# Optimization experiments

Hardware: AMD Instinct MI355X
Metric: run time of the kernel (lower is better)

The kernel has to match this reference:

```python
import jax, jax.numpy as jnp
import numpy as np

T_STEPS = 64   # fixed number of decode steps (original loops until depot is sampled)
CLIP_C = 10.0  # clip_c init arg


def setup_inputs() -> dict:
    key = jax.random.key(0)
    ks = jax.random.split(key, 8)
    B, N, E = 256, 1024, 256
    s = 0.02
    x = jax.random.normal(ks[0], (B, N, E), jnp.float32)
    demand = jax.random.uniform(ks[1], (B, N), jnp.float32) * 0.1
    demand = demand.at[:, 0].set(0.0)  # depot has zero demand
    capacity0 = jnp.full((B,), 5.0, jnp.float32)
    Wc = jax.random.normal(ks[2], (2 * E + 1, E), jnp.float32) * s
    bc = jnp.zeros((E,), jnp.float32)
    Wqkv = jax.random.normal(ks[3], (E, 3 * E), jnp.float32) * s
    bqkv = jnp.zeros((3 * E,), jnp.float32)
    Wo = jax.random.normal(ks[4], (E, E), jnp.float32) * s
    bo = jnp.zeros((E,), jnp.float32)
    Wpq = jax.random.normal(ks[5], (E, E), jnp.float32) * s
    bpq = jnp.zeros((E,), jnp.float32)
    Wpk = jax.random.normal(ks[6], (E, E), jnp.float32) * s
    bpk = jnp.zeros((E,), jnp.float32)
    return dict(x=x, demand=demand, capacity0=capacity0, Wc=Wc, bc=bc,
                Wqkv=Wqkv, bqkv=bqkv, Wo=Wo, bo=bo,
                Wpq=Wpq, bpq=bpq, Wpk=Wpk, bpk=bpk, num_heads=8)


def _decode(x, demand, capacity0, Wc, bc, Wqkv, bqkv, Wo, bo, Wpq, bpq, Wpk, bpk, num_heads):
    B, N, E = x.shape
    dh = E // num_heads
    scale = np.float32(1.0 / np.sqrt(dh))
    Wq_in, Wk_in, Wv_in = jnp.split(Wqkv, 3, axis=1)
    bq_in, bk_in, bv_in = jnp.split(bqkv, 3)
    # keys/values over static node embeddings: compute once (same math as per-step recompute)
    k_in = (x @ Wk_in + bk_in).reshape(B, N, num_heads, dh)
    v_in = (x @ Wv_in + bv_in).reshape(B, N, num_heads, dh)
    kp = x @ Wpk + bpk  # [B,N,E] pointer keys
    node_ids = jnp.arange(N)

    def step(carry, _):
        visited, current, capacity = carry
        # make_vehicle_embed (torch.no_grad -> stop_gradient)
        w = (~visited).astype(x.dtype)
        mean_embed = jax.lax.stop_gradient((x * w[:, :, None]).sum(1) / w.sum(1, keepdims=True))
        sel = jax.lax.stop_gradient(jnp.take_along_axis(x, current[:, None, None], axis=1)[:, 0])
        cap = jax.lax.stop_gradient(capacity)[:, None]
        ve = jnp.concatenate([mean_embed, sel, cap], axis=1) @ Wc + bc  # [B,E]
        # make_attn_mask: visited or demand > capacity; depot masked while at depot; unmask depot if all masked
        m = visited | (demand > capacity[:, None])
        m = m.at[:, 0].set(jnp.where(current == 0, True, m[:, 0]))
        m = m.at[:, 0].set(jnp.where(jnp.all(m, axis=1), False, m[:, 0]))
        # single-query MHA with key_padding_mask
        q = (ve @ Wq_in + bq_in).reshape(B, num_heads, dh)
        scores = jnp.einsum('bhd,bnhd->bhn', q, k_in) * scale
        attn = jax.nn.softmax(jnp.where(m[:, None, :], -jnp.inf, scores), axis=-1)
        ctx = jnp.einsum('bhn,bnhd->bhd', attn, v_in).reshape(B, E) @ Wo + bo  # [B,E]
        # ProbLayer: clipped-tanh masked softmax
        qp = ctx @ Wpq + bpq
        u = CLIP_C * jnp.tanh(jnp.einsum('bd,bnd->bn', qp, kp))
        prob = jax.nn.softmax(jnp.where(m, -jnp.inf, u), axis=-1)  # [B,N]
        # greedy selection + update_info
        node = jnp.argmax(prob, axis=-1).astype(jnp.int32)
        capacity = capacity - jnp.take_along_axis(demand, node[:, None].astype(jnp.int32), 1)[:, 0]
        visited = visited | ((node_ids[None, :] == node[:, None]) & (node != 0)[:, None])
        return (visited, node, capacity), (prob, node)

    init = (jnp.zeros((B, N), bool), jnp.zeros((B,), jnp.int32), capacity0)
    _, (probs, route) = jax.lax.scan(step, init, None, length=T_STEPS)
    return probs, route  # probs [T,B,N], route [T,B]


def reference(x, demand, capacity0, Wc, bc, Wqkv, bqkv, Wo, bo, Wpq, bpq, Wpk, bpk, num_heads):
    return _decode(x, demand, capacity0, Wc, bc, Wqkv, bqkv, Wo, bo, Wpq, bpq, Wpk, bpk, num_heads)
```

## Files before the change

### kernel.cpp

```cpp
#include <hip/hip_runtime.h>
#include <math.h>

#define BQ 256
#define NN 1024
#define EE 256
#define HH 8
#define TS 64
#define SCALE 0.17677669529663687f
#define CLIPC 10.0f

__global__ __launch_bounds__(256) void init_kernel(
    const float* __restrict__ x, const float* __restrict__ cap0,
    float* __restrict__ sum_embed, float* __restrict__ cnt,
    float* __restrict__ capb, int* __restrict__ curb,
    unsigned char* __restrict__ visited)
{
    int b = blockIdx.x, tid = threadIdx.x;
    #pragma unroll
    for (int i = 0; i < 4; i++) visited[b * NN + tid + i * 256] = 0;
    if (tid == 0) { cnt[b] = 1024.0f; capb[b] = cap0[b]; curb[b] = 0; }
    const float* xb = x + (size_t)b * NN * EE + tid;
    float s = 0.f;
    #pragma unroll 8
    for (int n = 0; n < NN; n++) s += xb[(size_t)n * EE];
    sum_embed[b * EE + tid] = s;
}

__global__ __launch_bounds__(512) void step_kernel(
    const float* __restrict__ x, const float* __restrict__ demand,
    const float* __restrict__ Wc, const float* __restrict__ bc,
    const float* __restrict__ Wqkv, const float* __restrict__ bqkv,
    const float* __restrict__ Wo, const float* __restrict__ bo,
    const float* __restrict__ Wpq, const float* __restrict__ bpq,
    const float* __restrict__ Wpk, const float* __restrict__ bpk,
    float* __restrict__ sum_embed, float* __restrict__ cntb,
    float* __restrict__ capb, int* __restrict__ curb,
    unsigned char* __restrict__ visited,
    float* __restrict__ probs_out, float* __restrict__ route_out, int t)
{
    __shared__ __align__(16) float xs[32768];
    __shared__ __align__(16) float g8[2048];
    __shared__ __align__(16) float ptl[8][16][8];
    __shared__ unsigned char masksh[NN];
    __shared__ float cvec[513];
    __shared__ float vevec[EE];
    __shared__ __align__(16) float qvec[EE];
    __shared__ float ctxv[EE];
    __shared__ float cov[EE];
    __shared__ __align__(16) float qpv[EE];
    __shared__ float uvec[NN];
    __shared__ float skk[512];
    __shared__ float mw_s[64], sw_s[64];
    __shared__ float MM[HH], SS[HH];
    __shared__ float red[8];
    __shared__ int   redi[8];
    __shared__ float s_mx, s_sum, s_ubias;
    __shared__ int   s_node;

    int b = blockIdx.x, tid = threadIdx.x;
    int w = tid >> 6, l = tid & 63;
    float capv = capb[b];
    int cur = curb[b];
    const float* xb = x + (size_t)b * NN * EE;

    {
        uchar2 vis = *(const uchar2*)(visited + b * NN + tid * 2);
        float2 dem = *(const float2*)(demand + b * NN + tid * 2);
        bool m0 = (vis.x != 0) || (dem.x > capv);
        bool m1 = (vis.y != 0) || (dem.y > capv);
        if (tid == 0 && cur == 0) m0 = true;
        masksh[tid * 2]     = m0 ? 1 : 0;
        masksh[tid * 2 + 1] = m1 ? 1 : 0;
        int allm = __syncthreads_and((m0 && m1) ? 1 : 0);
        if (allm && tid == 0) masksh[0] = 0;
    }
    if (tid < EE) {
        cvec[tid]      = sum_embed[b * EE + tid] / cntb[b];
        cvec[EE + tid] = xb[(size_t)cur * EE + tid];
    }
    if (tid == 0) cvec[512] = capv;
    __syncthreads();
    {
        int c = tid & 255, half = tid >> 8;
        int i0 = half * 256, i1 = half ? 513 : 256;
        float acc = 0.f;
        #pragma unroll 8
        for (int i = i0; i < i1; i++) acc = fmaf(cvec[i], Wc[i * EE + c], acc);
        skk[tid] = acc;
        __syncthreads();
        if (tid < EE) vevec[tid] = skk[tid] + skk[256 + tid] + bc[tid];
        __syncthreads();
    }
    {
        int c = tid & 255, half = tid >> 8;
        float acc = 0.f;
        #pragma unroll 8
        for (int i = half * 128; i < half * 128 + 128; i++)
            acc = fmaf(vevec[i], Wqkv[(size_t)i * 768 + c], acc);
        skk[tid] = acc;
        __syncthreads();
        if (tid < EE) qvec[tid] = skk[tid] + skk[256 + tid] + bqkv[tid];
        __syncthreads();
    }
    {
        int e = tid & 255, half = tid >> 8;
        const float* wr = Wqkv + (size_t)e * 768 + 256 + half * 128;
        const float* qh = qvec + half * 128;
        float a4[4] = {0.f, 0.f, 0.f, 0.f};
        #pragma unroll
        for (int k = 0; k < 32; k++) {
            float4 wv = *(const float4*)(wr + k * 4);
            float4 q4 = *(const float4*)(qh + k * 4);
            a4[k >> 3] = fmaf(wv.x, q4.x, fmaf(wv.y, q4.y,
                         fmaf(wv.z, q4.z, fmaf(wv.w, q4.w, a4[k >> 3]))));
        }
        #pragma unroll
        for (int hh2 = 0; hh2 < 4; hh2++)
            g8[(half * 4 + hh2) * EE + e] = SCALE * a4[hh2];
    }
    __syncthreads();

    float* xw = xs + w * 4096;
    int qtr = l >> 4, r = l & 15;
    float wsv[8][4] = {};
    float mrun[8], srun[8];
    #pragma unroll
    for (int h = 0; h < 8; h++) { mrun[h] = -INFINITY; srun[h] = 0.f; }

    for (int tt = 0; tt < 8; tt++) {
        int n0 = (w + tt * 8) * 16;
        float4 stg[16];
        #pragma unroll
        for (int i = 0; i < 16; i++)
            stg[i] = *(const float4*)(xb + (size_t)(n0 + i) * EE + l * 4);
        #pragma unroll
        for (int i = 0; i < 16; i++)
            *(float4*)(xw + i * 256 + ((l ^ (i & 7)) << 2)) = stg[i];
        float sacc[8] = {0.f, 0.f, 0.f, 0.f, 0.f, 0.f, 0.f, 0.f};
        #pragma unroll
        for (int gi = 0; gi < 16; gi++) {
            int c = qtr * 16 + ((gi + 2 * qtr) & 15);
            float4 xv = *(const float4*)(xw + r * 256 + ((c ^ (r & 7)) << 2));
            #pragma unroll
            for (int h = 0; h < 8; h++) {
                float4 gv = *(const float4*)(g8 + h * EE + (c << 2));
                sacc[h] = fmaf(xv.x, gv.x, fmaf(xv.y, gv.y,
                          fmaf(xv.z, gv.z, fmaf(xv.w, gv.w, sacc[h]))));
            }
        }
        int n = n0 + r;
        bool msk = masksh[n] != 0;
        float ptv[8], fac[8];
        #pragma unroll
        for (int h = 0; h < 8; h++) {
            float v = sacc[h];
            v += __shfl_xor(v, 16);
            v += __shfl_xor(v, 32);
            v = msk ? -INFINITY : v;
            float tm = v;
            tm = fmaxf(tm, __shfl_xor(tm, 1));
            tm = fmaxf(tm, __shfl_xor(tm, 2));
            tm = fmaxf(tm, __shfl_xor(tm, 4));
            tm = fmaxf(tm, __shfl_xor(tm, 8));
            float mo = mrun[h];
            float mn = fmaxf(mo, tm);
            float f  = (mo == -INFINITY) ? 0.f : expf(mo - mn);
            float pt = msk ? 0.f : expf(v - mn);
            float tsum = pt;
            tsum += __shfl_xor(tsum, 1);
            tsum += __shfl_xor(tsum, 2);
            tsum += __shfl_xor(tsum, 4);
            tsum += __shfl_xor(tsum, 8);
            srun[h] = fmaf(srun[h], f, tsum);
            mrun[h] = mn;
            fac[h] = f; ptv[h] = pt;
        }
        #pragma unroll
        for (int h = 0; h < 8; h++) {
            wsv[h][0] *= fac[h]; wsv[h][1] *= fac[h];
            wsv[h][2] *= fac[h]; wsv[h][3] *= fac[h];
        }
        if (qtr == 0) {
            *(float4*)&ptl[w][r][0] = make_float4(ptv[0], ptv[1], ptv[2], ptv[3]);
            *(float4*)&ptl[w][r][4] = make_float4(ptv[4], ptv[5], ptv[6], ptv[7]);
        }
        #pragma unroll
        for (int nd = 0; nd < 16; nd++) {
            float4 xv = *(const float4*)(xw + nd * 256 + ((l ^ (nd & 7)) << 2));
            float4 pa = *(const float4*)&ptl[w][nd][0];
            float4 pb = *(const float4*)&ptl[w][nd][4];
#define WSACC(H, P) \
            wsv[H][0] = fmaf(P, xv.x, wsv[H][0]); \
            wsv[H][1] = fmaf(P, xv.y, wsv[H][1]); \
            wsv[H][2] = fmaf(P, xv.z, wsv[H][2]); \
            wsv[H][3] = fmaf(P, xv.w, wsv[H][3]);
            WSACC(0, pa.x) WSACC(1, pa.y) WSACC(2, pa.z) WSACC(3, pa.w)
            WSACC(4, pb.x) WSACC(5, pb.y) WSACC(6, pb.z) WSACC(7, pb.w)
#undef WSACC
        }
    }
    if (l == 0) {
        #pragma unroll
        for (int h = 0; h < 8; h++) { mw_s[w * 8 + h] = mrun[h]; sw_s[w * 8 + h] = srun[h]; }
    }
    __syncthreads();
    if (tid < 8) {
        float M = -INFINITY;
        for (int w2 = 0; w2 < 8; w2++) M = fmaxf(M, mw_s[w2 * 8 + tid]);
        float S = 0.f;
        for (int w2 = 0; w2 < 8; w2++) {
            float mm = mw_s[w2 * 8 + tid];
            if (mm > -INFINITY) S += sw_s[w2 * 8 + tid] * expf(mm - M);
        }
        MM[tid] = M; SS[tid] = S;
    }
    __syncthreads();
    #pragma unroll
    for (int h = 0; h < 8; h++) {
        float mm = mrun[h];
        float f = (mm > -INFINITY) ? expf(mm - MM[h]) : 0.f;
        *(float4*)(xs + (w * 8 + h) * 256 + l * 4) =
            make_float4(wsv[h][0] * f, wsv[h][1] * f, wsv[h][2] * f, wsv[h][3] * f);
    }
    __syncthreads();
    #pragma unroll
    for (int k = 0; k < 4; k++) {
        int idx = tid + k * 512;
        float s = 0.f;
        #pragma unroll
        for (int w2 = 0; w2 < 8; w2++) s += xs[w2 * 2048 + idx];
        g8[idx] = s;
    }
    __syncthreads();

    {
        int c = tid & 255, half = tid >> 8;
        int h2 = c >> 5;
        const float* wv = Wqkv + 512 + c;
        float acc = 0.f;
        #pragma unroll 8
        for (int e = half * 128; e < half * 128 + 128; e++)
            acc = fmaf(g8[h2 * EE + e], wv[(size_t)e * 768], acc);
        skk[tid] = acc;
        __syncthreads();
        if (tid < EE) ctxv[tid] = (skk[tid] + skk[256 + tid]) / SS[tid >> 5] + bqkv[512 + tid];
        __syncthreads();
    }
    {
        int c = tid & 255, half = tid >> 8;
        float acc = 0.f;
        #pragma unroll 8
        for (int i = half * 128; i < half * 128 + 128; i++)
            acc = fmaf(ctxv[i], Wo[(size_t)i * EE + c], acc);
        skk[tid] = acc;
        __syncthreads();
        if (tid < EE) cov[tid] = skk[tid] + skk[256 + tid] + bo[tid];
        __syncthreads();
    }
    {
        int c = tid & 255, half = tid >> 8;
        float acc = 0.f;
        #pragma unroll 8
        for (int i = half * 128; i < half * 128 + 128; i++)
            acc = fmaf(cov[i], Wpq[(size_t)i * EE + c], acc);
        skk[tid] = acc;
        __syncthreads();
        if (tid < EE) qpv[tid] = skk[tid] + skk[256 + tid] + bpq[tid];
        __syncthreads();
    }
    {
        float v = (tid < EE) ? qpv[tid] * bpk[tid] : 0.f;
        #pragma unroll
        for (int o = 32; o > 0; o >>= 1) v += __shfl_down(v, o);
        if (l == 0) red[w] = v;
        __syncthreads();
        if (tid == 0) {
            float s2 = 0.f;
            for (int i = 0; i < 8; i++) s2 += red[i];
            s_ubias = s2;
        }
    }
    {
        __syncthreads();
        int e = tid & 255, half = tid >> 8;
        const float* wr = Wpk + (size_t)e * EE + half * 128;
        const float* qh = qpv + half * 128;
        float acc = 0.f;
        #pragma unroll
        for (int k = 0; k < 32; k++) {
            float4 wv = *(const float4*)(wr + k * 4);
            float4 q4 = *(const float4*)(qh + k * 4);
            acc = fmaf(wv.x, q4.x, fmaf(wv.y, q4.y,
                  fmaf(wv.z, q4.z, fmaf(wv.w, q4.w, acc))));
        }
        skk[tid] = acc;
        __syncthreads();
        if (tid < EE) g8[tid] = skk[tid] + skk[256 + tid];
        __syncthreads();
    }

    float ubias = s_ubias;
    for (int tt = 0; tt < 8; tt++) {
        int n0 = (w + tt * 8) * 16;
        float4 stg[16];
        #pragma unroll
        for (int i = 0; i < 16; i++)
            stg[i] = *(const float4*)(xb + (size_t)(n0 + i) * EE + l * 4);
        #pragma unroll
        for (int i = 0; i < 16; i++)
            *(float4*)(xw + i * 256 + ((l ^ (i & 7)) << 2)) = stg[i];
        float acc = 0.f;
        #pragma unroll
        for (int gi = 0; gi < 16; gi++) {
            int c = qtr * 16 + ((gi + 2 * qtr) & 15);
            float4 xv = *(const float4*)(xw + r * 256 + ((c ^ (r & 7)) << 2));
            float4 hv = *(const float4*)(g8 + (c << 2));
            acc = fmaf(xv.x, hv.x, fmaf(xv.y, hv.y,
                  fmaf(xv.z, hv.z, fmaf(xv.w, hv.w, acc))));
        }
        acc += __shfl_xor(acc, 16);
        acc += __shfl_xor(acc, 32);
        if (qtr == 0) {
            int n = n0 + r;
            uvec[n] = masksh[n] ? -INFINITY : CLIPC * tanhf(acc + ubias);
        }
    }
    __syncthreads();

    float u0 = uvec[tid], u1 = uvec[tid + 512];
    float lmax = fmaxf(u0, u1);
    #pragma unroll
    for (int o = 32; o > 0; o >>= 1) lmax = fmaxf(lmax, __shfl_down(lmax, o));
    if (l == 0) red[w] = lmax;
    __syncthreads();
    if (tid == 0) {
        float m2 = red[0];
        for (int i = 1; i < 8; i++) m2 = fmaxf(m2, red[i]);
        s_mx = m2;
    }
    __syncthreads();
    float mx = s_mx;
    float p0 = (u0 == -INFINITY) ? 0.f : expf(u0 - mx);
    float p1 = (u1 == -INFINITY) ? 0.f : expf(u1 - mx);
    float ls = p0 + p1;
    #pragma unroll
    for (int o = 32; o > 0; o >>= 1) ls += __shfl_down(ls, o);
    if (l == 0) red[w] = ls;
    __syncthreads();
    if (tid == 0) {
        float s2 = 0.f;
        for (int i = 0; i < 8; i++) s2 += red[i];
        s_sum = s2;
    }
    __syncthreads();
    float sm = s_sum;
    p0 = p0 / sm; p1 = p1 / sm;
    size_t pbase = (size_t)t * BQ * NN + (size_t)b * NN;
    probs_out[pbase + tid] = p0;
    probs_out[pbase + tid + 512] = p1;
    float bu; int bn;
    if (p1 > p0) { bu = p1; bn = tid + 512; } else { bu = p0; bn = tid; }
    #pragma unroll
    for (int o = 32; o > 0; o >>= 1) {
        float ou = __shfl_down(bu, o);
        int   on = __shfl_down(bn, o);
        if (ou > bu || (ou == bu && on < bn)) { bu = ou; bn = on; }
    }
    if (l == 0) { red[w] = bu; redi[w] = bn; }
    __syncthreads();
    if (tid == 0) {
        float vv = red[0]; int nd = redi[0];
        for (int i = 1; i < 8; i++)
            if (red[i] > vv || (red[i] == vv && redi[i] < nd)) { vv = red[i]; nd = redi[i]; }
        s_node = nd;
        route_out[t * BQ + b] = (float)nd;
        capb[b] = capv - demand[b * NN + nd];
        curb[b] = nd;
        if (nd != 0) { visited[b * NN + nd] = 1; cntb[b] -= 1.f; }
    }
    __syncthreads();
    int node = s_node;
    if (node != 0 && tid < EE)
        sum_embed[b * EE + tid] -= xb[(size_t)node * EE + tid];
}

extern "C" void kernel_launch(void* const* d_in, const int* in_sizes, int n_in,
                              void* d_out, int out_size, void* d_ws, size_t ws_size,
                              hipStream_t stream) {
    const float* x      = (const float*)d_in[0];
    const float* demand = (const float*)d_in[1];
    const float* cap0   = (const float*)d_in[2];
    const float* Wc     = (const float*)d_in[3];
    const float* bc     = (const float*)d_in[4];
    const float* Wqkv   = (const float*)d_in[5];
    const float* bqkv   = (const float*)d_in[6];
    const float* Wo     = (const float*)d_in[7];
    const float* bo     = (const float*)d_in[8];
    const float* Wpq    = (const float*)d_in[9];
    const float* bpq    = (const float*)d_in[10];
    const float* Wpk    = (const float*)d_in[11];
    const float* bpk    = (const float*)d_in[12];
    float* out = (float*)d_out;

    float* sum_embed = (float*)d_ws;
    float* cnt       = sum_embed + 65536;
    float* capbuf    = cnt + 256;
    int*   curbuf    = (int*)(capbuf + 256);
    unsigned char* visited = (unsigned char*)(curbuf + 256);

    float* probs_out = out;
    float* route_out = out + (size_t)TS * BQ * NN;

    hipLaunchKernelGGL(init_kernel, dim3(BQ), dim3(256), 0, stream,
                       x, cap0, sum_embed, cnt, capbuf, curbuf, visited);
    for (int t = 0; t < TS; t++) {
        hipLaunchKernelGGL(step_kernel, dim3(BQ), dim3(512), 0, stream,
                           x, demand, Wc, bc, Wqkv, bqkv, Wo, bo, Wpq, bpq,
                           Wpk, bpk, sum_embed, cnt, capbuf, curbuf, visited,
                           probs_out, route_out, t);
    }
}
```

Baseline: 18.44 ms.

## Double step kernel to 1024 threads with 8-node tiles and shuffle-based pointer scores

Raises the per-batch step kernel from 512 to 1024 threads (16 waves). Each wave now handles 8-node tiles, and all the small matvecs are split four ways. The attention value accumulation reuses register-staged x instead of re-reading shared memory, and the LDS swizzle is dropped. The pointer-key pass no longer stages x through LDS; it computes dot products directly and reduces them with a butterfly shuffle transpose. The goal is more memory-level parallelism per CU for the streaming x reads, at the cost of register pressure under 1024-thread launch bounds and possible LDS bank conflicts without the swizzle.

```diff
diff --git a/kernel.cpp b/kernel.cpp
--- a/kernel.cpp
+++ b/kernel.cpp
@@ -26,7 +26,7 @@
     sum_embed[b * EE + tid] = s;
 }
 
-__global__ __launch_bounds__(512) void step_kernel(
+__global__ __launch_bounds__(1024) void step_kernel(
     const float* __restrict__ x, const float* __restrict__ demand,
     const float* __restrict__ Wc, const float* __restrict__ bc,
     const float* __restrict__ Wqkv, const float* __restrict__ bqkv,
@@ -40,20 +40,19 @@
 {
     __shared__ __align__(16) float xs[32768];
     __shared__ __align__(16) float g8[2048];
-    __shared__ __align__(16) float ptl[8][16][8];
+    __shared__ __align__(16) float ptlu[1024];
     __shared__ unsigned char masksh[NN];
     __shared__ float cvec[513];
     __shared__ float vevec[EE];
-    __shared__ __align__(16) float qvec[EE];
+    __shared__ __align__(16) float qvec_s[EE];
     __shared__ float ctxv[EE];
     __shared__ float cov[EE];
-    __shared__ __align__(16) float qpv[EE];
-    __shared__ float uvec[NN];
-    __shared__ float skk[512];
-    __shared__ float mw_s[64], sw_s[64];
+    __shared__ __align__(16) float qpv_s[EE];
+    __shared__ __align__(16) float skk[1024];
+    __shared__ float mw_s[128], sw_s[128];
     __shared__ float MM[HH], SS[HH];
-    __shared__ float red[8];
-    __shared__ int   redi[8];
+    __shared__ float red[16];
+    __shared__ int   redi[16];
     __shared__ float s_mx, s_sum, s_ubias;
     __shared__ int   s_node;
 
@@ -64,14 +63,12 @@
     const float* xb = x + (size_t)b * NN * EE;
 
     {
-        uchar2 vis = *(const uchar2*)(visited + b * NN + tid * 2);
-        float2 dem = *(const float2*)(demand + b * NN + tid * 2);
-        bool m0 = (vis.x != 0) || (dem.x > capv);
-        bool m1 = (vis.y != 0) || (dem.y > capv);
+        unsigned char vis = visited[b * NN + tid];
+        float dm = demand[b * NN + tid];
+        bool m0 = (vis != 0) || (dm > capv);
         if (tid == 0 && cur == 0) m0 = true;
-        masksh[tid * 2]     = m0 ? 1 : 0;
-        masksh[tid * 2 + 1] = m1 ? 1 : 0;
-        int allm = __syncthreads_and((m0 && m1) ? 1 : 0);
+        masksh[tid] = m0 ? 1 : 0;
+        int allm = __syncthreads_and(m0 ? 1 : 0);
         if (allm && tid == 0) masksh[0] = 0;
     }
     if (tid < EE) {
@@ -81,79 +78,78 @@
     if (tid == 0) cvec[512] = capv;
     __syncthreads();
     {
-        int c = tid & 255, half = tid >> 8;
-        int i0 = half * 256, i1 = half ? 513 : 256;
+        int c = tid & 255, q = tid >> 8;
+        int i0 = q * 128, i1 = (q == 3) ? 513 : i0 + 128;
         float acc = 0.f;
         #pragma unroll 8
-        for (int i = i0; i < i1; i++) acc = fmaf(cvec[i], Wc[i * EE + c], acc);
-        skk[tid] = acc;
-        __syncthreads();
-        if (tid < EE) vevec[tid] = skk[tid] + skk[256 + tid] + bc[tid];
-        __syncthreads();
-    }
-    {
-        int c = tid & 255, half = tid >> 8;
+        for (int i = i0; i < i1; i++) acc = fmaf(cvec[i], Wc[(size_t)i * EE + c], acc);
+        skk[tid] = acc;
+        __syncthreads();
+        if (tid < EE) vevec[tid] = skk[tid] + skk[tid + 256] + skk[tid + 512] + skk[tid + 768] + bc[tid];
+        __syncthreads();
+    }
+    {
+        int c = tid & 255, q = tid >> 8;
         float acc = 0.f;
         #pragma unroll 8
-        for (int i = half * 128; i < half * 128 + 128; i++)
+        for (int i = q * 64; i < q * 64 + 64; i++)
             acc = fmaf(vevec[i], Wqkv[(size_t)i * 768 + c], acc);
         skk[tid] = acc;
         __syncthreads();
-        if (tid < EE) qvec[tid] = skk[tid] + skk[256 + tid] + bqkv[tid];
-        __syncthreads();
-    }
-    {
-        int e = tid & 255, half = tid >> 8;
-        const float* wr = Wqkv + (size_t)e * 768 + 256 + half * 128;
-        const float* qh = qvec + half * 128;
-        float a4[4] = {0.f, 0.f, 0.f, 0.f};
-        #pragma unroll
-        for (int k = 0; k < 32; k++) {
+        if (tid < EE) qvec_s[tid] = skk[tid] + skk[tid + 256] + skk[tid + 512] + skk[tid + 768] + bqkv[tid];
+        __syncthreads();
+    }
+    {
+        int e = tid & 255, q = tid >> 8;
+        const float* wr = Wqkv + (size_t)e * 768 + 256 + q * 64;
+        const float* qh = qvec_s + q * 64;
+        float a2[2] = {0.f, 0.f};
+        #pragma unroll
+        for (int k = 0; k < 16; k++) {
             float4 wv = *(const float4*)(wr + k * 4);
             float4 q4 = *(const float4*)(qh + k * 4);
-            a4[k >> 3] = fmaf(wv.x, q4.x, fmaf(wv.y, q4.y,
-                         fmaf(wv.z, q4.z, fmaf(wv.w, q4.w, a4[k >> 3]))));
-        }
-        #pragma unroll
-        for (int hh2 = 0; hh2 < 4; hh2++)
-            g8[(half * 4 + hh2) * EE + e] = SCALE * a4[hh2];
-    }
-    __syncthreads();
-
-    float* xw = xs + w * 4096;
-    int qtr = l >> 4, r = l & 15;
+            a2[k >> 3] = fmaf(wv.x, q4.x, fmaf(wv.y, q4.y,
+                         fmaf(wv.z, q4.z, fmaf(wv.w, q4.w, a2[k >> 3]))));
+        }
+        g8[(2 * q + 0) * EE + e] = SCALE * a2[0];
+        g8[(2 * q + 1) * EE + e] = SCALE * a2[1];
+    }
+    __syncthreads();
+
+    float* xw = xs + w * 2048;
+    int oct = l >> 3, r = l & 7;
     float wsv[8][4] = {};
     float mrun[8], srun[8];
     #pragma unroll
     for (int h = 0; h < 8; h++) { mrun[h] = -INFINITY; srun[h] = 0.f; }
 
     for (int tt = 0; tt < 8; tt++) {
-        int n0 = (w + tt * 8) * 16;
-        float4 stg[16];
-        #pragma unroll
-        for (int i = 0; i < 16; i++)
+        int n0 = (w + tt * 16) * 8;
+        float4 stg[8];
+        #pragma unroll
+        for (int i = 0; i < 8; i++)
             stg[i] = *(const float4*)(xb + (size_t)(n0 + i) * EE + l * 4);
         #pragma unroll
-        for (int i = 0; i < 16; i++)
-            *(float4*)(xw + i * 256 + ((l ^ (i & 7)) << 2)) = stg[i];
+        for (int i = 0; i < 8; i++)
+            *(float4*)(xw + i * 256 + l * 4) = stg[i];
         float sacc[8] = {0.f, 0.f, 0.f, 0.f, 0.f, 0.f, 0.f, 0.f};
         #pragma unroll
-        for (int gi = 0; gi < 16; gi++) {
-            int c = qtr * 16 + ((gi + 2 * qtr) & 15);
-            float4 xv = *(const float4*)(xw + r * 256 + ((c ^ (r & 7)) << 2));
+        for (int gi = 0; gi < 8; gi++) {
+            int c = oct * 8 + ((gi + oct) & 7);
+            float4 xv = *(const float4*)(xw + r * 256 + c * 4);
             #pragma unroll
             for (int h = 0; h < 8; h++) {
-                float4 gv = *(const float4*)(g8 + h * EE + (c << 2));
+                float4 gv = *(const float4*)(g8 + h * EE + c * 4);
                 sacc[h] = fmaf(xv.x, gv.x, fmaf(xv.y, gv.y,
                           fmaf(xv.z, gv.z, fmaf(xv.w, gv.w, sacc[h]))));
             }
         }
         int n = n0 + r;
         bool msk = masksh[n] != 0;
-        float ptv[8], fac[8];
         #pragma unroll
         for (int h = 0; h < 8; h++) {
             float v = sacc[h];
+            v += __shfl_xor(v, 8);
             v += __shfl_xor(v, 16);
             v += __shfl_xor(v, 32);
             v = msk ? -INFINITY : v;
@@ -161,34 +157,24 @@
             tm = fmaxf(tm, __shfl_xor(tm, 1));
             tm = fmaxf(tm, __shfl_xor(tm, 2));
             tm = fmaxf(tm, __shfl_xor(tm, 4));
-            tm = fmaxf(tm, __shfl_xor(tm, 8));
             float mo = mrun[h];
             float mn = fmaxf(mo, tm);
             float f  = (mo == -INFINITY) ? 0.f : expf(mo - mn);
             float pt = msk ? 0.f : expf(v - mn);
-            float tsum = pt;
-            tsum += __shfl_xor(tsum, 1);
-            tsum += __shfl_xor(tsum, 2);
-            tsum += __shfl_xor(tsum, 4);
-            tsum += __shfl_xor(tsum, 8);
-            srun[h] = fmaf(srun[h], f, tsum);
+            float ts = pt;
+            ts += __shfl_xor(ts, 1);
+            ts += __shfl_xor(ts, 2);
+            ts += __shfl_xor(ts, 4);
+            srun[h] = fmaf(srun[h], f, ts);
             mrun[h] = mn;
-            fac[h] = f; ptv[h] = pt;
-        }
-        #pragma unroll
-        for (int h = 0; h < 8; h++) {
-            wsv[h][0] *= fac[h]; wsv[h][1] *= fac[h];
-            wsv[h][2] *= fac[h]; wsv[h][3] *= fac[h];
-        }
-        if (qtr == 0) {
-            *(float4*)&ptl[w][r][0] = make_float4(ptv[0], ptv[1], ptv[2], ptv[3]);
-            *(float4*)&ptl[w][r][4] = make_float4(ptv[4], ptv[5], ptv[6], ptv[7]);
-        }
-        #pragma unroll
-        for (int nd = 0; nd < 16; nd++) {
-            float4 xv = *(const float4*)(xw + nd * 256 + ((l ^ (nd & 7)) << 2));
-            float4 pa = *(const float4*)&ptl[w][nd][0];
-            float4 pb = *(const float4*)&ptl[w][nd][4];
+            if (oct == 0) ptlu[w * 64 + r * 8 + h] = pt;
+            wsv[h][0] *= f; wsv[h][1] *= f; wsv[h][2] *= f; wsv[h][3] *= f;
+        }
+        #pragma unroll
+        for (int nd = 0; nd < 8; nd++) {
+            float4 pa = *(const float4*)(ptlu + w * 64 + nd * 8);
+            float4 pb = *(const float4*)(ptlu + w * 64 + nd * 8 + 4);
+            float4 xv = stg[nd];
 #define WSACC(H, P) \
             wsv[H][0] = fmaf(P, xv.x, wsv[H][0]); \
             wsv[H][1] = fmaf(P, xv.y, wsv[H][1]); \
@@ -206,9 +192,9 @@
     __syncthreads();
     if (tid < 8) {
         float M = -INFINITY;
-        for (int w2 = 0; w2 < 8; w2++) M = fmaxf(M, mw_s[w2 * 8 + tid]);
+        for (int w2 = 0; w2 < 16; w2++) M = fmaxf(M, mw_s[w2 * 8 + tid]);
         float S = 0.f;
-        for (int w2 = 0; w2 < 8; w2++) {
+        for (int w2 = 0; w2 < 16; w2++) {
             float mm = mw_s[w2 * 8 + tid];
             if (mm > -INFINITY) S += sw_s[w2 * 8 + tid] * expf(mm - M);
         }
@@ -219,75 +205,74 @@
     for (int h = 0; h < 8; h++) {
         float mm = mrun[h];
         float f = (mm > -INFINITY) ? expf(mm - MM[h]) : 0.f;
-        *(float4*)(xs + (w * 8 + h) * 256 + l * 4) =
+        *(float4*)(xs + w * 2048 + h * 256 + l * 4) =
             make_float4(wsv[h][0] * f, wsv[h][1] * f, wsv[h][2] * f, wsv[h][3] * f);
     }
     __syncthreads();
     #pragma unroll
-    for (int k = 0; k < 4; k++) {
-        int idx = tid + k * 512;
+    for (int k = 0; k < 2; k++) {
+        int idx = tid + k * 1024;
         float s = 0.f;
         #pragma unroll
-        for (int w2 = 0; w2 < 8; w2++) s += xs[w2 * 2048 + idx];
+        for (int w2 = 0; w2 < 16; w2++) s += xs[w2 * 2048 + idx];
         g8[idx] = s;
     }
     __syncthreads();
 
     {
-        int c = tid & 255, half = tid >> 8;
+        int c = tid & 255, q = tid >> 8;
         int h2 = c >> 5;
         const float* wv = Wqkv + 512 + c;
         float acc = 0.f;
         #pragma unroll 8
-        for (int e = half * 128; e < half * 128 + 128; e++)
+        for (int e = q * 64; e < q * 64 + 64; e++)
             acc = fmaf(g8[h2 * EE + e], wv[(size_t)e * 768], acc);
         skk[tid] = acc;
         __syncthreads();
-        if (tid < EE) ctxv[tid] = (skk[tid] + skk[256 + tid]) / SS[tid >> 5] + bqkv[512 + tid];
-        __syncthreads();
-    }
-    {
-        int c = tid & 255, half = tid >> 8;
+        if (tid < EE) ctxv[tid] = (skk[tid] + skk[tid + 256] + skk[tid + 512] + skk[tid + 768]) / SS[tid >> 5] + bqkv[512 + tid];
+        __syncthreads();
+    }
+    {
+        int c = tid & 255, q = tid >> 8;
         float acc = 0.f;
         #pragma unroll 8
-        for (int i = half * 128; i < half * 128 + 128; i++)
+        for (int i = q * 64; i < q * 64 + 64; i++)
             acc = fmaf(ctxv[i], Wo[(size_t)i * EE + c], acc);
         skk[tid] = acc;
         __syncthreads();
-        if (tid < EE) cov[tid] = skk[tid] + skk[256 + tid] + bo[tid];
-        __syncthreads();
-    }
-    {
-        int c = tid & 255, half = tid >> 8;
+        if (tid < EE) cov[tid] = skk[tid] + skk[tid + 256] + skk[tid + 512] + skk[tid + 768] + bo[tid];
+        __syncthreads();
+    }
+    {
+        int c = tid & 255, q = tid >> 8;
         float acc = 0.f;
         #pragma unroll 8
-        for (int i = half * 128; i < half * 128 + 128; i++)
+        for (int i = q * 64; i < q * 64 + 64; i++)
             acc = fmaf(cov[i], Wpq[(size_t)i * EE + c], acc);
         skk[tid] = acc;
         __syncthreads();
-        if (tid < EE) qpv[tid] = skk[tid] + skk[256 + tid] + bpq[tid];
-        __syncthreads();
-    }
-    {
-        float v = (tid < EE) ? qpv[tid] * bpk[tid] : 0.f;
-        #pragma unroll
-        for (int o = 32; o > 0; o >>= 1) v += __shfl_down(v, o);
-        if (l == 0) red[w] = v;
+        if (tid < EE) qpv_s[tid] = skk[tid] + skk[tid + 256] + skk[tid + 512] + skk[tid + 768] + bpq[tid];
+        __syncthreads();
+    }
+    {
+        float vv = (tid < EE) ? qpv_s[tid] * bpk[tid] : 0.f;
+        #pragma unroll
+        for (int o = 32; o > 0; o >>= 1) vv += __shfl_down(vv, o);
+        if (l == 0) red[w] = vv;
         __syncthreads();
         if (tid == 0) {
             float s2 = 0.f;
-            for (int i = 0; i < 8; i++) s2 += red[i];
+            for (int i = 0; i < 16; i++) s2 += red[i];
             s_ubias = s2;
         }
     }
     {
-        __syncthreads();
-        int e = tid & 255, half = tid >> 8;
-        const float* wr = Wpk + (size_t)e * EE + half * 128;
-        const float* qh = qpv + half * 128;
-        float acc = 0.f;
-        #pragma unroll
-        for (int k = 0; k < 32; k++) {
+        int e = tid & 255, q = tid >> 8;
+        const float* wr = Wpk + (size_t)e * EE + q * 64;
+        const float* qh = qpv_s + q * 64;
+        float acc = 0.f;
+        #pragma unroll
+        for (int k = 0; k < 16; k++) {
             float4 wv = *(const float4*)(wr + k * 4);
             float4 q4 = *(const float4*)(qh + k * 4);
             acc = fmaf(wv.x, q4.x, fmaf(wv.y, q4.y,
@@ -295,71 +280,87 @@
         }
         skk[tid] = acc;
         __syncthreads();
-        if (tid < EE) g8[tid] = skk[tid] + skk[256 + tid];
+        if (tid < EE) g8[tid] = skk[tid] + skk[tid + 256] + skk[tid + 512] + skk[tid + 768];
         __syncthreads();
     }
 
     float ubias = s_ubias;
+    float4 ht4 = *(const float4*)(g8 + l * 4);
     for (int tt = 0; tt < 8; tt++) {
-        int n0 = (w + tt * 8) * 16;
-        float4 stg[16];
-        #pragma unroll
-        for (int i = 0; i < 16; i++)
-            stg[i] = *(const float4*)(xb + (size_t)(n0 + i) * EE + l * 4);
-        #pragma unroll
-        for (int i = 0; i < 16; i++)
-            *(float4*)(xw + i * 256 + ((l ^ (i & 7)) << 2)) = stg[i];
-        float acc = 0.f;
-        #pragma unroll
-        for (int gi = 0; gi < 16; gi++) {
-            int c = qtr * 16 + ((gi + 2 * qtr) & 15);
-            float4 xv = *(const float4*)(xw + r * 256 + ((c ^ (r & 7)) << 2));
-            float4 hv = *(const float4*)(g8 + (c << 2));
-            acc = fmaf(xv.x, hv.x, fmaf(xv.y, hv.y,
-                  fmaf(xv.z, hv.z, fmaf(xv.w, hv.w, acc))));
-        }
-        acc += __shfl_xor(acc, 16);
-        acc += __shfl_xor(acc, 32);
-        if (qtr == 0) {
-            int n = n0 + r;
-            uvec[n] = masksh[n] ? -INFINITY : CLIPC * tanhf(acc + ubias);
-        }
-    }
-    __syncthreads();
-
-    float u0 = uvec[tid], u1 = uvec[tid + 512];
-    float lmax = fmaxf(u0, u1);
+        int n0 = (w + tt * 16) * 8;
+        float pacc[8];
+        #pragma unroll
+        for (int i = 0; i < 8; i++) {
+            float4 sg = *(const float4*)(xb + (size_t)(n0 + i) * EE + l * 4);
+            pacc[i] = fmaf(sg.x, ht4.x, fmaf(sg.y, ht4.y, fmaf(sg.z, ht4.z, sg.w * ht4.w)));
+        }
+        #pragma unroll
+        for (int i = 0; i < 8; i++) {
+            pacc[i] += __shfl_xor(pacc[i], 8);
+            pacc[i] += __shfl_xor(pacc[i], 16);
+            pacc[i] += __shfl_xor(pacc[i], 32);
+        }
+        float b0, b1, b2, b3;
+        {
+            float e0, o0;
+            e0 = (l & 1) ? pacc[1] : pacc[0]; o0 = (l & 1) ? pacc[0] : pacc[1];
+            b0 = e0 + __shfl_xor(o0, 1);
+            e0 = (l & 1) ? pacc[3] : pacc[2]; o0 = (l & 1) ? pacc[2] : pacc[3];
+            b1 = e0 + __shfl_xor(o0, 1);
+            e0 = (l & 1) ? pacc[5] : pacc[4]; o0 = (l & 1) ? pacc[4] : pacc[5];
+            b2 = e0 + __shfl_xor(o0, 1);
+            e0 = (l & 1) ? pacc[7] : pacc[6]; o0 = (l & 1) ? pacc[6] : pacc[7];
+            b3 = e0 + __shfl_xor(o0, 1);
+        }
+        float c0, c1;
+        {
+            float e0 = (l & 2) ? b1 : b0, o0 = (l & 2) ? b0 : b1;
+            c0 = e0 + __shfl_xor(o0, 2);
+            e0 = (l & 2) ? b3 : b2; o0 = (l & 2) ? b2 : b3;
+            c1 = e0 + __shfl_xor(o0, 2);
+        }
+        float d0;
+        {
+            float e0 = (l & 4) ? c1 : c0, o0 = (l & 4) ? c0 : c1;
+            d0 = e0 + __shfl_xor(o0, 4);
+        }
+        if (l < 8) {
+            int n = n0 + l;
+            ptlu[n] = masksh[n] ? -INFINITY : CLIPC * tanhf(d0 + ubias);
+        }
+    }
+    __syncthreads();
+
+    float u0 = ptlu[tid];
+    float lmax = u0;
     #pragma unroll
     for (int o = 32; o > 0; o >>= 1) lmax = fmaxf(lmax, __shfl_down(lmax, o));
     if (l == 0) red[w] = lmax;
     __syncthreads();
     if (tid == 0) {
         float m2 = red[0];
-        for (int i = 1; i < 8; i++) m2 = fmaxf(m2, red[i]);
+        for (int i = 1; i < 16; i++) m2 = fmaxf(m2, red[i]);
         s_mx = m2;
     }
     __syncthreads();
     float mx = s_mx;
     float p0 = (u0 == -INFINITY) ? 0.f : expf(u0 - mx);
-    float p1 = (u1 == -INFINITY) ? 0.f : expf(u1 - mx);
-    float ls = p0 + p1;
+    float ls = p0;
     #pragma unroll
     for (int o = 32; o > 0; o >>= 1) ls += __shfl_down(ls, o);
     if (l == 0) red[w] = ls;
     __syncthreads();
     if (tid == 0) {
         float s2 = 0.f;
-        for (int i = 0; i < 8; i++) s2 += red[i];
+        for (int i = 0; i < 16; i++) s2 += red[i];
         s_sum = s2;
     }
     __syncthreads();
     float sm = s_sum;
-    p0 = p0 / sm; p1 = p1 / sm;
+    p0 = p0 / sm;
     size_t pbase = (size_t)t * BQ * NN + (size_t)b * NN;
     probs_out[pbase + tid] = p0;
-    probs_out[pbase + tid + 512] = p1;
-    float bu; int bn;
-    if (p1 > p0) { bu = p1; bn = tid + 512; } else { bu = p0; bn = tid; }
+    float bu = p0; int bn = tid;
     #pragma unroll
     for (int o = 32; o > 0; o >>= 1) {
         float ou = __shfl_down(bu, o);
@@ -369,9 +370,9 @@
     if (l == 0) { red[w] = bu; redi[w] = bn; }
     __syncthreads();
     if (tid == 0) {
-        float vv = red[0]; int nd = redi[0];
-        for (int i = 1; i < 8; i++)
-            if (red[i] > vv || (red[i] == vv && redi[i] < nd)) { vv = red[i]; nd = redi[i]; }
+        float vv2 = red[0]; int nd = redi[0];
+        for (int i = 1; i < 16; i++)
+            if (red[i] > vv2 || (red[i] == vv2 && redi[i] < nd)) { vv2 = red[i]; nd = redi[i]; }
         s_node = nd;
         route_out[t * BQ + b] = (float)nd;
         capb[b] = capv - demand[b * NN + nd];
@@ -414,7 +415,7 @@
     hipLaunchKernelGGL(init_kernel, dim3(BQ), dim3(256), 0, stream,
                        x, cap0, sum_embed, cnt, capbuf, curbuf, visited);
     for (int t = 0; t < TS; t++) {
-        hipLaunchKernelGGL(step_kernel, dim3(BQ), dim3(512), 0, stream,
+        hipLaunchKernelGGL(step_kernel, dim3(BQ), dim3(1024), 0, stream,
                            x, demand, Wc, bc, Wqkv, bqkv, Wo, bo, Wpq, bpq,
                            Wpk, bpk, sum_embed, cnt, capbuf, curbuf, visited,
                            probs_out, route_out, t);
```

After: 46.47 ms. +152.0%, slower.

## Double-buffer x tiles via direct global-to-LDS loads in attention and pointer passes

Applied to the files above, without the earlier changes.

Replaces the register-staged loads of x into shared memory with direct global-to-LDS loads (global_load_lds), double-buffered in 8-row chunks per wave so the next chunk streams in while the current one is computed. The first chunk is prefetched early to overlap with the small matvecs. The pointer-logit pass is restructured with a butterfly shuffle reduction, and the uvec/ptl buffers are merged to free shared memory. This adds manual waitcnt and sched_barrier control and drops the XOR swizzle, which may introduce LDS bank conflicts.

```diff
diff --git a/kernel.cpp b/kernel.cpp
--- a/kernel.cpp
+++ b/kernel.cpp
@@ -8,6 +8,11 @@
 #define TS 64
 #define SCALE 0.17677669529663687f
 #define CLIPC 10.0f
+
+#define GLD16(gp, lp)                                                         \
+    __builtin_amdgcn_global_load_lds(                                         \
+        (const __attribute__((address_space(1))) void*)(gp),                  \
+        (__attribute__((address_space(3))) void*)(lp), 16, 0, 0)
 
 __global__ __launch_bounds__(256) void init_kernel(
     const float* __restrict__ x, const float* __restrict__ cap0,
@@ -40,16 +45,15 @@
 {
     __shared__ __align__(16) float xs[32768];
     __shared__ __align__(16) float g8[2048];
-    __shared__ __align__(16) float ptl[8][16][8];
+    __shared__ __align__(16) float ptlu[1024];
     __shared__ unsigned char masksh[NN];
     __shared__ float cvec[513];
     __shared__ float vevec[EE];
-    __shared__ __align__(16) float qvec[EE];
+    __shared__ __align__(16) float qvec_s[EE];
     __shared__ float ctxv[EE];
     __shared__ float cov[EE];
-    __shared__ __align__(16) float qpv[EE];
-    __shared__ float uvec[NN];
-    __shared__ float skk[512];
+    __shared__ __align__(16) float qpv_s[EE];
+    __shared__ __align__(16) float skk[512];
     __shared__ float mw_s[64], sw_s[64];
     __shared__ float MM[HH], SS[HH];
     __shared__ float red[8];
@@ -62,6 +66,8 @@
     float capv = capb[b];
     int cur = curb[b];
     const float* xb = x + (size_t)b * NN * EE;
+    float* buf0 = xs + w * 2048;
+    float* buf1 = xs + 16384 + w * 2048;
 
     {
         uchar2 vis = *(const uchar2*)(visited + b * NN + tid * 2);
@@ -74,6 +80,12 @@
         int allm = __syncthreads_and((m0 && m1) ? 1 : 0);
         if (allm && tid == 0) masksh[0] = 0;
     }
+    {
+        int n0 = w * 8;
+        #pragma unroll
+        for (int i = 0; i < 8; i++)
+            GLD16(xb + (size_t)(n0 + i) * EE + l * 4, buf0 + i * 256);
+    }
     if (tid < EE) {
         cvec[tid]      = sum_embed[b * EE + tid] / cntb[b];
         cvec[EE + tid] = xb[(size_t)cur * EE + tid];
@@ -85,7 +97,7 @@
         int i0 = half * 256, i1 = half ? 513 : 256;
         float acc = 0.f;
         #pragma unroll 8
-        for (int i = i0; i < i1; i++) acc = fmaf(cvec[i], Wc[i * EE + c], acc);
+        for (int i = i0; i < i1; i++) acc = fmaf(cvec[i], Wc[(size_t)i * EE + c], acc);
         skk[tid] = acc;
         __syncthreads();
         if (tid < EE) vevec[tid] = skk[tid] + skk[256 + tid] + bc[tid];
@@ -99,13 +111,13 @@
             acc = fmaf(vevec[i], Wqkv[(size_t)i * 768 + c], acc);
         skk[tid] = acc;
         __syncthreads();
-        if (tid < EE) qvec[tid] = skk[tid] + skk[256 + tid] + bqkv[tid];
+        if (tid < EE) qvec_s[tid] = skk[tid] + skk[256 + tid] + bqkv[tid];
         __syncthreads();
     }
     {
         int e = tid & 255, half = tid >> 8;
         const float* wr = Wqkv + (size_t)e * 768 + 256 + half * 128;
-        const float* qh = qvec + half * 128;
+        const float* qh = qvec_s + half * 128;
         float a4[4] = {0.f, 0.f, 0.f, 0.f};
         #pragma unroll
         for (int k = 0; k < 32; k++) {
@@ -120,75 +132,69 @@
     }
     __syncthreads();
 
-    float* xw = xs + w * 4096;
-    int qtr = l >> 4, r = l & 15;
+    int r = l >> 3, oct = l & 7;
     float wsv[8][4] = {};
     float mrun[8], srun[8];
     #pragma unroll
     for (int h = 0; h < 8; h++) { mrun[h] = -INFINITY; srun[h] = 0.f; }
 
-    for (int tt = 0; tt < 8; tt++) {
-        int n0 = (w + tt * 8) * 16;
-        float4 stg[16];
-        #pragma unroll
-        for (int i = 0; i < 16; i++)
-            stg[i] = *(const float4*)(xb + (size_t)(n0 + i) * EE + l * 4);
-        #pragma unroll
-        for (int i = 0; i < 16; i++)
-            *(float4*)(xw + i * 256 + ((l ^ (i & 7)) << 2)) = stg[i];
+    for (int tt = 0; tt < 16; tt++) {
+        const float* curb_ = (tt & 1) ? buf1 : buf0;
+        float* nxtb = (tt & 1) ? buf0 : buf1;
+        if (tt < 15) {
+            int nn0 = (w + (tt + 1) * 8) * 8;
+            #pragma unroll
+            for (int i = 0; i < 8; i++)
+                GLD16(xb + (size_t)(nn0 + i) * EE + l * 4, nxtb + i * 256);
+            asm volatile("s_waitcnt vmcnt(8)" ::: "memory");
+        } else {
+            asm volatile("s_waitcnt vmcnt(0)" ::: "memory");
+        }
+        __builtin_amdgcn_sched_barrier(0);
+        int n0 = (w + tt * 8) * 8;
         float sacc[8] = {0.f, 0.f, 0.f, 0.f, 0.f, 0.f, 0.f, 0.f};
         #pragma unroll
-        for (int gi = 0; gi < 16; gi++) {
-            int c = qtr * 16 + ((gi + 2 * qtr) & 15);
-            float4 xv = *(const float4*)(xw + r * 256 + ((c ^ (r & 7)) << 2));
+        for (int gi = 0; gi < 8; gi++) {
+            int c = oct * 8 + ((gi + oct) & 7);
+            float4 xv = *(const float4*)(curb_ + r * 256 + c * 4);
             #pragma unroll
             for (int h = 0; h < 8; h++) {
-                float4 gv = *(const float4*)(g8 + h * EE + (c << 2));
+                float4 gv = *(const float4*)(g8 + h * EE + c * 4);
                 sacc[h] = fmaf(xv.x, gv.x, fmaf(xv.y, gv.y,
                           fmaf(xv.z, gv.z, fmaf(xv.w, gv.w, sacc[h]))));
             }
         }
         int n = n0 + r;
         bool msk = masksh[n] != 0;
-        float ptv[8], fac[8];
         #pragma unroll
         for (int h = 0; h < 8; h++) {
             float v = sacc[h];
-            v += __shfl_xor(v, 16);
-            v += __shfl_xor(v, 32);
+            v += __shfl_xor(v, 1);
+            v += __shfl_xor(v, 2);
+            v += __shfl_xor(v, 4);
             v = msk ? -INFINITY : v;
             float tm = v;
-            tm = fmaxf(tm, __shfl_xor(tm, 1));
-            tm = fmaxf(tm, __shfl_xor(tm, 2));
-            tm = fmaxf(tm, __shfl_xor(tm, 4));
             tm = fmaxf(tm, __shfl_xor(tm, 8));
+            tm = fmaxf(tm, __shfl_xor(tm, 16));
+            tm = fmaxf(tm, __shfl_xor(tm, 32));
             float mo = mrun[h];
             float mn = fmaxf(mo, tm);
             float f  = (mo == -INFINITY) ? 0.f : expf(mo - mn);
             float pt = msk ? 0.f : expf(v - mn);
-            float tsum = pt;
-            tsum += __shfl_xor(tsum, 1);
-            tsum += __shfl_xor(tsum, 2);
-            tsum += __shfl_xor(tsum, 4);
-            tsum += __shfl_xor(tsum, 8);
-            srun[h] = fmaf(srun[h], f, tsum);
+            float ts = pt;
+            ts += __shfl_xor(ts, 8);
+            ts += __shfl_xor(ts, 16);
+            ts += __shfl_xor(ts, 32);
+            srun[h] = fmaf(srun[h], f, ts);
             mrun[h] = mn;
-            fac[h] = f; ptv[h] = pt;
-        }
-        #pragma unroll
-        for (int h = 0; h < 8; h++) {
-            wsv[h][0] *= fac[h]; wsv[h][1] *= fac[h];
-            wsv[h][2] *= fac[h]; wsv[h][3] *= fac[h];
-        }
-        if (qtr == 0) {
-            *(float4*)&ptl[w][r][0] = make_float4(ptv[0], ptv[1], ptv[2], ptv[3]);
-            *(float4*)&ptl[w][r][4] = make_float4(ptv[4], ptv[5], ptv[6], ptv[7]);
-        }
-        #pragma unroll
-        for (int nd = 0; nd < 16; nd++) {
-            float4 xv = *(const float4*)(xw + nd * 256 + ((l ^ (nd & 7)) << 2));
-            float4 pa = *(const float4*)&ptl[w][nd][0];
-            float4 pb = *(const float4*)&ptl[w][nd][4];
+            if (oct == 0) ptlu[w * 64 + r * 8 + h] = pt;
+            wsv[h][0] *= f; wsv[h][1] *= f; wsv[h][2] *= f; wsv[h][3] *= f;
+        }
+        #pragma unroll
+        for (int nd = 0; nd < 8; nd++) {
+            float4 xv = *(const float4*)(curb_ + nd * 256 + l * 4);
+            float4 pa = *(const float4*)(ptlu + w * 64 + nd * 8);
+            float4 pb = *(const float4*)(ptlu + w * 64 + nd * 8 + 4);
 #define WSACC(H, P) \
             wsv[H][0] = fmaf(P, xv.x, wsv[H][0]); \
             wsv[H][1] = fmaf(P, xv.y, wsv[H][1]); \
@@ -232,6 +238,12 @@
         g8[idx] = s;
     }
     __syncthreads();
+    {
+        int n0 = w * 8;
+        #pragma unroll
+        for (int i = 0; i < 8; i++)
+            GLD16(xb + (size_t)(n0 + i) * EE + l * 4, buf0 + i * 256);
+    }
 
     {
         int c = tid & 255, half = tid >> 8;
@@ -265,14 +277,14 @@
             acc = fmaf(cov[i], Wpq[(size_t)i * EE + c], acc);
         skk[tid] = acc;
         __syncthreads();
-        if (tid < EE) qpv[tid] = skk[tid] + skk[256 + tid] + bpq[tid];
-        __syncthreads();
-    }
-    {
-        float v = (tid < EE) ? qpv[tid] * bpk[tid] : 0.f;
-        #pragma unroll
-        for (int o = 32; o > 0; o >>= 1) v += __shfl_down(v, o);
-        if (l == 0) red[w] = v;
+        if (tid < EE) qpv_s[tid] = skk[tid] + skk[256 + tid] + bpq[tid];
+        __syncthreads();
+    }
+    {
+        float vv = (tid < EE) ? qpv_s[tid] * bpk[tid] : 0.f;
+        #pragma unroll
+        for (int o = 32; o > 0; o >>= 1) vv += __shfl_down(vv, o);
+        if (l == 0) red[w] = vv;
         __syncthreads();
         if (tid == 0) {
             float s2 = 0.f;
@@ -281,10 +293,9 @@
         }
     }
     {
-        __syncthreads();
         int e = tid & 255, half = tid >> 8;
         const float* wr = Wpk + (size_t)e * EE + half * 128;
-        const float* qh = qpv + half * 128;
+        const float* qh = qpv_s + half * 128;
         float acc = 0.f;
         #pragma unroll
         for (int k = 0; k < 32; k++) {
@@ -300,34 +311,65 @@
     }
 
     float ubias = s_ubias;
-    for (int tt = 0; tt < 8; tt++) {
-        int n0 = (w + tt * 8) * 16;
-        float4 stg[16];
-        #pragma unroll
-        for (int i = 0; i < 16; i++)
-            stg[i] = *(const float4*)(xb + (size_t)(n0 + i) * EE + l * 4);
-        #pragma unroll
-        for (int i = 0; i < 16; i++)
-            *(float4*)(xw + i * 256 + ((l ^ (i & 7)) << 2)) = stg[i];
-        float acc = 0.f;
-        #pragma unroll
-        for (int gi = 0; gi < 16; gi++) {
-            int c = qtr * 16 + ((gi + 2 * qtr) & 15);
-            float4 xv = *(const float4*)(xw + r * 256 + ((c ^ (r & 7)) << 2));
-            float4 hv = *(const float4*)(g8 + (c << 2));
-            acc = fmaf(xv.x, hv.x, fmaf(xv.y, hv.y,
-                  fmaf(xv.z, hv.z, fmaf(xv.w, hv.w, acc))));
-        }
-        acc += __shfl_xor(acc, 16);
-        acc += __shfl_xor(acc, 32);
-        if (qtr == 0) {
-            int n = n0 + r;
-            uvec[n] = masksh[n] ? -INFINITY : CLIPC * tanhf(acc + ubias);
-        }
-    }
-    __syncthreads();
-
-    float u0 = uvec[tid], u1 = uvec[tid + 512];
+    float4 ht4 = *(const float4*)(g8 + l * 4);
+    for (int tt = 0; tt < 16; tt++) {
+        const float* curb_ = (tt & 1) ? buf1 : buf0;
+        float* nxtb = (tt & 1) ? buf0 : buf1;
+        if (tt < 15) {
+            int nn0 = (w + (tt + 1) * 8) * 8;
+            #pragma unroll
+            for (int i = 0; i < 8; i++)
+                GLD16(xb + (size_t)(nn0 + i) * EE + l * 4, nxtb + i * 256);
+            asm volatile("s_waitcnt vmcnt(8)" ::: "memory");
+        } else {
+            asm volatile("s_waitcnt vmcnt(0)" ::: "memory");
+        }
+        __builtin_amdgcn_sched_barrier(0);
+        int n0 = (w + tt * 8) * 8;
+        float pacc[8];
+        #pragma unroll
+        for (int i = 0; i < 8; i++) {
+            float4 sg = *(const float4*)(curb_ + i * 256 + l * 4);
+            pacc[i] = fmaf(sg.x, ht4.x, fmaf(sg.y, ht4.y, fmaf(sg.z, ht4.z, sg.w * ht4.w)));
+        }
+        #pragma unroll
+        for (int i = 0; i < 8; i++) {
+            pacc[i] += __shfl_xor(pacc[i], 8);
+            pacc[i] += __shfl_xor(pacc[i], 16);
+            pacc[i] += __shfl_xor(pacc[i], 32);
+        }
+        float b0, b1, b2, b3;
+        {
+            float e0, o0;
+            e0 = (l & 1) ? pacc[1] : pacc[0]; o0 = (l & 1) ? pacc[0] : pacc[1];
+            b0 = e0 + __shfl_xor(o0, 1);
+            e0 = (l & 1) ? pacc[3] : pacc[2]; o0 = (l & 1) ? pacc[2] : pacc[3];
+            b1 = e0 + __shfl_xor(o0, 1);
+            e0 = (l & 1) ? pacc[5] : pacc[4]; o0 = (l & 1) ? pacc[4] : pacc[5];
+            b2 = e0 + __shfl_xor(o0, 1);
+            e0 = (l & 1) ? pacc[7] : pacc[6]; o0 = (l & 1) ? pacc[6] : pacc[7];
+            b3 = e0 + __shfl_xor(o0, 1);
+        }
+        float c0, c1;
+        {
+            float e0 = (l & 2) ? b1 : b0, o0 = (l & 2) ? b0 : b1;
+            c0 = e0 + __shfl_xor(o0, 2);
+            e0 = (l & 2) ? b3 : b2; o0 = (l & 2) ? b2 : b3;
+            c1 = e0 + __shfl_xor(o0, 2);
+        }
+        float d0;
+        {
+            float e0 = (l & 4) ? c1 : c0, o0 = (l & 4) ? c0 : c1;
+            d0 = e0 + __shfl_xor(o0, 4);
+        }
+        if (l < 8) {
+            int n = n0 + l;
+            ptlu[n] = masksh[n] ? -INFINITY : CLIPC * tanhf(d0 + ubias);
+        }
+    }
+    __syncthreads();
+
+    float u0 = ptlu[tid], u1 = ptlu[tid + 512];
     float lmax = fmaxf(u0, u1);
     #pragma unroll
     for (int o = 32; o > 0; o >>= 1) lmax = fmaxf(lmax, __shfl_down(lmax, o));
@@ -369,9 +411,9 @@
     if (l == 0) { red[w] = bu; redi[w] = bn; }
     __syncthreads();
     if (tid == 0) {
-        float vv = red[0]; int nd = redi[0];
+        float vv2 = red[0]; int nd = redi[0];
         for (int i = 1; i < 8; i++)
-            if (red[i] > vv || (red[i] == vv && redi[i] < nd)) { vv = red[i]; nd = redi[i]; }
+            if (red[i] > vv2 || (red[i] == vv2 && redi[i] < nd)) { vv2 = red[i]; nd = redi[i]; }
         s_node = nd;
         route_out[t * BQ + b] = (float)nd;
         capb[b] = capv - demand[b * NN + nd];
```

Result: slower. 32.87 ms (+78.2%).
